# Kernel optimization log

Hardware: AMD Instinct MI355X
Metric: run time of the kernel (lower is better)

The kernel has to match this reference:

```python
import jax, jax.numpy as jnp
import numpy as np

N = 50000      # nodes
E = 1600000    # edges (avg degree 32)
DIN, DH, DOUT = 256, 128, 64


def gcn_conv(x, W, b, row, col, w, n):
    """One GCNConv layer (self-loops already appended to row/col/w).
    row = source nodes, col = target nodes; aggregate at targets."""
    xw = x @ W                                        # [n, d_out]
    deg = jax.ops.segment_sum(w, col, num_segments=n)  # in-degree weighted
    dinv = jnp.where(deg > 0, jax.lax.rsqrt(deg), 0.0)
    norm = dinv[row] * w * dinv[col]                  # [E+n]
    msg = norm[:, None] * xw[row]                     # [E+n, d_out] gather
    out = jax.ops.segment_sum(msg, col, num_segments=n)
    return out + b


def setup_inputs() -> dict:
    key = jax.random.key(0)
    k = jax.random.split(key, 6)
    x = jax.random.normal(k[0], (N, DIN), dtype=jnp.float32)
    edge_index = jax.random.randint(k[1], (2, E), 0, N)
    edge_weight = jax.random.uniform(k[2], (E,), dtype=jnp.float32)
    W1 = jax.random.normal(k[3], (DIN, DH), dtype=jnp.float32) * (1.0 / np.sqrt(DIN))
    b1 = jnp.zeros((DH,), dtype=jnp.float32)
    W2 = jax.random.normal(k[4], (DH, DOUT), dtype=jnp.float32) * (1.0 / np.sqrt(DH))
    b2 = jnp.zeros((DOUT,), dtype=jnp.float32)
    return {"x": x, "edge_index": edge_index, "edge_weight": edge_weight,
            "W1": W1, "b1": b1, "W2": W2, "b2": b2}


def reference(x, edge_index, edge_weight, W1, b1, W2, b2):
    n = x.shape[0]
    loops = jnp.arange(n, dtype=edge_index.dtype)
    row = jnp.concatenate([edge_index[0], loops])
    col = jnp.concatenate([edge_index[1], loops])
    w = jnp.concatenate([edge_weight, jnp.ones((n,), dtype=edge_weight.dtype)])
    h = gcn_conv(x, W1, b1, row, col, w, n)
    h = jax.nn.relu(h)
    # dropout(p=0.2) is identity in eval mode
    h = gcn_conv(h, W2, b2, row, col, w, n)
    return jax.nn.log_softmax(h, axis=-1)
```

## Files before the change

### kernel.cpp

```cpp
#include <hip/hip_runtime.h>
#include <hip/hip_bf16.h>
#include <cstddef>


#define DIN 256
#define DH  128
#define DOUT 64
#define NPB 100
#define NBMAX 512

typedef __bf16 bf16x8 __attribute__((ext_vector_type(8)));
typedef float f32x4 __attribute__((ext_vector_type(4)));

__device__ __forceinline__ float bflo(unsigned u) { return __uint_as_float(u << 16); }
__device__ __forceinline__ float bfhi(unsigned u) { return __uint_as_float(u & 0xffff0000u); }
__device__ __forceinline__ unsigned short f2bf(float f) {
    unsigned u = __float_as_uint(f);
    unsigned r = (u + 0x7fffu + ((u >> 16) & 1u)) >> 16;
    return (unsigned short)r;
}

__global__ void prep_w_kernel(const float* __restrict__ W1, const float* __restrict__ W2,
                              unsigned short* __restrict__ wt1, unsigned short* __restrict__ wt2) {
    int i = blockIdx.x * 256 + threadIdx.x;
    if (i < DH * DIN) {
        int nn = i >> 8, k = i & 255;
        wt1[i] = f2bf(W1[k * DH + nn]);
    } else {
        int j = i - DH * DIN;
        if (j < DOUT * DH) {
            int nn = j >> 7, k = j & 127;
            wt2[j] = f2bf(W2[k * DOUT + nn]);
        }
    }
}

__launch_bounds__(256)
__global__ void hist_kernel(const int* __restrict__ col, int* __restrict__ bh,
                            int E, int Ec, int NB) {
    __shared__ int hist[NBMAX];
    int p = blockIdx.x, t = threadIdx.x;
    for (int b = t; b < NB; b += 256) hist[b] = 0;
    __syncthreads();
    int s = p * Ec, e = min(s + Ec, E);
    for (int i = s + t; i < e; i += 256) atomicAdd(&hist[col[i] / NPB], 1);
    __syncthreads();
    for (int b = t; b < NB; b += 256) bh[p * NB + b] = hist[b];
}

__launch_bounds__(512)
__global__ void colscan_kernel(int* __restrict__ bh, int* __restrict__ btotal,
                               int P, int NB) {
    __shared__ int arr[512];
    int b = blockIdx.x, t = threadIdx.x;
    arr[t] = (t < P) ? bh[t * NB + b] : 0;
    __syncthreads();
    for (int off = 1; off < 512; off <<= 1) {
        int v = (t >= off) ? arr[t - off] : 0;
        __syncthreads();
        arr[t] += v;
        __syncthreads();
    }
    int excl = (t == 0) ? 0 : arr[t - 1];
    if (t < P) bh[t * NB + b] = excl;
    if (t == P - 1) btotal[b] = arr[t];
}

__launch_bounds__(512)
__global__ void basescan_kernel(const int* __restrict__ btotal, int* __restrict__ bbase,
                                int* __restrict__ rowptr, int NB, int n, int E) {
    __shared__ int arr[512];
    int t = threadIdx.x;
    arr[t] = (t < NB) ? btotal[t] : 0;
    __syncthreads();
    for (int off = 1; off < 512; off <<= 1) {
        int v = (t >= off) ? arr[t - off] : 0;
        __syncthreads();
        arr[t] += v;
        __syncthreads();
    }
    int excl = (t == 0) ? 0 : arr[t - 1];
    if (t <= NB) bbase[t] = excl;
    if (t == 511) rowptr[n] = E;
}

__launch_bounds__(256)
__global__ void scatter_kernel(const int* __restrict__ row, const int* __restrict__ col,
                               const float* __restrict__ w, const int* __restrict__ bh,
                               const int* __restrict__ bbase, int2* __restrict__ part,
                               int E, int Ec, int NB) {
    __shared__ int cur[NBMAX];
    int p = blockIdx.x, t = threadIdx.x;
    for (int b = t; b < NB; b += 256) cur[b] = bbase[b] + bh[p * NB + b];
    __syncthreads();
    int s = p * Ec, e = min(s + Ec, E);
    for (int i = s + t; i < e; i += 256) {
        int c = col[i];
        int r = row[i];
        int b = c / NPB;
        int pos = atomicAdd(&cur[b], 1);
        part[pos] = make_int2(r | ((c - b * NPB) << 16), __float_as_int(w[i]));
    }
}

__launch_bounds__(256)
__global__ void bucket_csr_kernel(const int2* __restrict__ part, const int* __restrict__ bbase,
                                  float* __restrict__ dinv, int* __restrict__ rowptr,
                                  int2* __restrict__ final_e, int n) {
    __shared__ int   hist[NPB];
    __shared__ float wsum[NPB];
    __shared__ int   nbase[NPB];
    __shared__ int   cur[NPB];
    int b = blockIdx.x, t = threadIdx.x;
    if (t < NPB) { hist[t] = 0; wsum[t] = 0.0f; }
    __syncthreads();
    int s = bbase[b], e = bbase[b + 1];
    for (int i = s + t; i < e; i += 256) {
        int2 rec = part[i];
        int cl = rec.x >> 16;
        atomicAdd(&hist[cl], 1);
        atomicAdd(&wsum[cl], __int_as_float(rec.y));
    }
    __syncthreads();
    if (t == 0) {
        int run = 0;
        for (int k = 0; k < NPB; ++k) { nbase[k] = run; run += hist[k]; }
    }
    __syncthreads();
    if (t < NPB) {
        int node = b * NPB + t;
        if (node < n) {
            dinv[node] = rsqrtf(1.0f + wsum[t]);
            rowptr[node] = s + nbase[t];
        }
        cur[t] = nbase[t];
    }
    __syncthreads();
    for (int i = s + t; i < e; i += 256) {
        int2 rec = part[i];
        int cl = rec.x >> 16;
        int q = s + atomicAdd(&cur[cl], 1);
        final_e[q] = make_int2(rec.x & 0xffff, rec.y);
    }
}

template <int K, int M>
__launch_bounds__(256)
__global__ void gemm_mfma_kernel(const float* __restrict__ A,
                                 const unsigned short* __restrict__ Wt,
                                 const float* __restrict__ scale,
                                 unsigned short* __restrict__ C, int N) {
    constexpr int BK = 64, LD = BK + 8;
    constexpr int WN = M / 4;
    constexpr int NT = WN / 16;
    constexpr int CLD = M + 8;
    constexpr int SM = (64 * LD + M * LD) > (64 * CLD) ? (64 * LD + M * LD) : (64 * CLD);
    __shared__ unsigned short smem[SM];
    __shared__ float sdv[64];
    unsigned short* As = smem;
    unsigned short* Bs = smem + 64 * LD;

    const int tid = threadIdx.x;
    const int row0 = blockIdx.x * 64;
    const int lane = tid & 63;
    const int quad = lane >> 4, r16 = lane & 15;
    const int n0 = (tid >> 6) * WN;

    if (tid < 64) {
        int r = row0 + tid;
        sdv[tid] = (r < N) ? scale[r] : 0.0f;
    }

    f32x4 acc[4][NT];
#pragma unroll
    for (int mt = 0; mt < 4; ++mt)
#pragma unroll
        for (int nt = 0; nt < NT; ++nt)
            acc[mt][nt] = (f32x4){0.f, 0.f, 0.f, 0.f};

    for (int k0 = 0; k0 < K; k0 += BK) {
#pragma unroll
        for (int j = 0; j < 4; ++j) {
            int idx = tid + j * 256;
            int m = idx >> 4;
            int q = idx & 15;
            int gr = row0 + m;
            float4 v = make_float4(0.f, 0.f, 0.f, 0.f);
            if (gr < N) v = *(const float4*)&A[(size_t)gr * K + k0 + q * 4];
            ushort4 s4;
            s4.x = f2bf(v.x); s4.y = f2bf(v.y); s4.z = f2bf(v.z); s4.w = f2bf(v.w);
            *(ushort4*)&As[m * LD + q * 4] = s4;
        }
#pragma unroll
        for (int j = 0; j < M * 8 / 256; ++j) {
            int idx = tid + j * 256;
            int nn = idx >> 3;
            int q = idx & 7;
            uint4 v = *(const uint4*)&Wt[(size_t)nn * K + k0 + q * 8];
            *(uint4*)&Bs[nn * LD + q * 8] = v;
        }
        __syncthreads();
#pragma unroll
        for (int ks = 0; ks < BK / 32; ++ks) {
            bf16x8 af[4], bfr[NT];
#pragma unroll
            for (int nt = 0; nt < NT; ++nt)
                bfr[nt] = *(const bf16x8*)&Bs[(n0 + nt * 16 + r16) * LD + ks * 32 + quad * 8];
#pragma unroll
            for (int mt = 0; mt < 4; ++mt)
                af[mt] = *(const bf16x8*)&As[(mt * 16 + r16) * LD + ks * 32 + quad * 8];
#pragma unroll
            for (int mt = 0; mt < 4; ++mt)
#pragma unroll
                for (int nt = 0; nt < NT; ++nt)
                    acc[mt][nt] = __builtin_amdgcn_mfma_f32_16x16x32_bf16(
                        af[mt], bfr[nt], acc[mt][nt], 0, 0, 0);
        }
        __syncthreads();
    }
    unsigned short* Cs = smem;
#pragma unroll
    for (int mt = 0; mt < 4; ++mt) {
#pragma unroll
        for (int i = 0; i < 4; ++i) {
            int r = mt * 16 + quad * 4 + i;
            float sc = sdv[r];
#pragma unroll
            for (int nt = 0; nt < NT; ++nt)
                Cs[r * CLD + n0 + nt * 16 + r16] = f2bf(acc[mt][nt][i] * sc);
        }
    }
    __syncthreads();
#pragma unroll
    for (int j = 0; j < 64 * M / 8 / 256; ++j) {
        int idx = tid + j * 256;
        int r = idx / (M / 8);
        int q = idx % (M / 8);
        int gr = row0 + r;
        if (gr < N) {
            uint4 v = *(const uint4*)&Cs[r * CLD + q * 8];
            *(uint4*)&C[(size_t)gr * M + q * 8] = v;
        }
    }
}

__launch_bounds__(256)
__global__ void agg1_kernel(const uint2* __restrict__ xw,
                            const int* __restrict__ rowptr,
                            const int2* __restrict__ edge,
                            const float* __restrict__ dinv,
                            const float* __restrict__ bias,
                            float* __restrict__ out, int n) {
    int node = blockIdx.x * 4 + (threadIdx.x >> 6);
    if (node >= n) return;
    int lane = threadIdx.x & 63;
    int half = lane >> 5, sub = lane & 31;
    float a0 = 0.f, a1 = 0.f, a2 = 0.f, a3 = 0.f;
    if (half == 0) {
        uint2 u = xw[(size_t)node * 32 + sub];
        a0 = bflo(u.x); a1 = bfhi(u.x); a2 = bflo(u.y); a3 = bfhi(u.y);
    }
    int p = rowptr[node], p1 = rowptr[node + 1];
    for (; p + 8 <= p1; p += 8) {
        int2 e0 = edge[p + half],     e1 = edge[p + 2 + half];
        int2 e2 = edge[p + 4 + half], e3 = edge[p + 6 + half];
        uint2 v0 = xw[(size_t)e0.x * 32 + sub];
        uint2 v1 = xw[(size_t)e1.x * 32 + sub];
        uint2 v2 = xw[(size_t)e2.x * 32 + sub];
        uint2 v3 = xw[(size_t)e3.x * 32 + sub];
        float w0 = __int_as_float(e0.y), w1 = __int_as_float(e1.y);
        float w2 = __int_as_float(e2.y), w3 = __int_as_float(e3.y);
        a0 += w0 * bflo(v0.x) + w1 * bflo(v1.x) + w2 * bflo(v2.x) + w3 * bflo(v3.x);
        a1 += w0 * bfhi(v0.x) + w1 * bfhi(v1.x) + w2 * bfhi(v2.x) + w3 * bfhi(v3.x);
        a2 += w0 * bflo(v0.y) + w1 * bflo(v1.y) + w2 * bflo(v2.y) + w3 * bflo(v3.y);
        a3 += w0 * bfhi(v0.y) + w1 * bfhi(v1.y) + w2 * bfhi(v2.y) + w3 * bfhi(v3.y);
    }
    for (; p + 2 <= p1; p += 2) {
        int2 e0 = edge[p + half];
        uint2 v0 = xw[(size_t)e0.x * 32 + sub];
        float w0 = __int_as_float(e0.y);
        a0 += w0 * bflo(v0.x); a1 += w0 * bfhi(v0.x);
        a2 += w0 * bflo(v0.y); a3 += w0 * bfhi(v0.y);
    }
    if (p < p1 && half == 0) {
        int2 e0 = edge[p];
        uint2 v0 = xw[(size_t)e0.x * 32 + sub];
        float w0 = __int_as_float(e0.y);
        a0 += w0 * bflo(v0.x); a1 += w0 * bfhi(v0.x);
        a2 += w0 * bflo(v0.y); a3 += w0 * bfhi(v0.y);
    }
    a0 += __shfl_xor(a0, 32); a1 += __shfl_xor(a1, 32);
    a2 += __shfl_xor(a2, 32); a3 += __shfl_xor(a3, 32);
    float di = dinv[node];
    float4 b = ((const float4*)bias)[sub];
    a0 = fmaxf(di * a0 + b.x, 0.f);
    a1 = fmaxf(di * a1 + b.y, 0.f);
    a2 = fmaxf(di * a2 + b.z, 0.f);
    a3 = fmaxf(di * a3 + b.w, 0.f);
    if (half == 0)
        ((float4*)out)[(size_t)node * 32 + sub] = make_float4(a0, a1, a2, a3);
}

__launch_bounds__(256)
__global__ void agg2_kernel(const uint2* __restrict__ xw,
                            const int* __restrict__ rowptr,
                            const int2* __restrict__ edge,
                            const float* __restrict__ dinv,
                            const float* __restrict__ bias,
                            float* __restrict__ out, int n) {
    int node = blockIdx.x * 4 + (threadIdx.x >> 6);
    if (node >= n) return;
    int lane = threadIdx.x & 63;
    int qw = lane >> 4, sub = lane & 15;
    float a0 = 0.f, a1 = 0.f, a2 = 0.f, a3 = 0.f;
    if (qw == 0) {
        uint2 u = xw[(size_t)node * 16 + sub];
        a0 = bflo(u.x); a1 = bfhi(u.x); a2 = bflo(u.y); a3 = bfhi(u.y);
    }
    int p = rowptr[node], p1 = rowptr[node + 1];
    for (; p + 8 <= p1; p += 8) {
        int2 e0 = edge[p + qw], e1 = edge[p + 4 + qw];
        uint2 v0 = xw[(size_t)e0.x * 16 + sub];
        uint2 v1 = xw[(size_t)e1.x * 16 + sub];
        float w0 = __int_as_float(e0.y), w1 = __int_as_float(e1.y);
        a0 += w0 * bflo(v0.x) + w1 * bflo(v1.x);
        a1 += w0 * bfhi(v0.x) + w1 * bfhi(v1.x);
        a2 += w0 * bflo(v0.y) + w1 * bflo(v1.y);
        a3 += w0 * bfhi(v0.y) + w1 * bfhi(v1.y);
    }
    for (; p + 4 <= p1; p += 4) {
        int2 e0 = edge[p + qw];
        uint2 v0 = xw[(size_t)e0.x * 16 + sub];
        float w0 = __int_as_float(e0.y);
        a0 += w0 * bflo(v0.x); a1 += w0 * bfhi(v0.x);
        a2 += w0 * bflo(v0.y); a3 += w0 * bfhi(v0.y);
    }
    int rem = p1 - p;
    if (qw < rem) {
        int2 e0 = edge[p + qw];
        uint2 v0 = xw[(size_t)e0.x * 16 + sub];
        float w0 = __int_as_float(e0.y);
        a0 += w0 * bflo(v0.x); a1 += w0 * bfhi(v0.x);
        a2 += w0 * bflo(v0.y); a3 += w0 * bfhi(v0.y);
    }
    a0 += __shfl_xor(a0, 32); a1 += __shfl_xor(a1, 32);
    a2 += __shfl_xor(a2, 32); a3 += __shfl_xor(a3, 32);
    a0 += __shfl_xor(a0, 16); a1 += __shfl_xor(a1, 16);
    a2 += __shfl_xor(a2, 16); a3 += __shfl_xor(a3, 16);
    float di = dinv[node];
    float4 b = ((const float4*)bias)[sub];
    a0 = di * a0 + b.x; a1 = di * a1 + b.y;
    a2 = di * a2 + b.z; a3 = di * a3 + b.w;
    float m = fmaxf(fmaxf(a0, a1), fmaxf(a2, a3));
#pragma unroll
    for (int off = 8; off > 0; off >>= 1) m = fmaxf(m, __shfl_xor(m, off));
    float s = __expf(a0 - m) + __expf(a1 - m) + __expf(a2 - m) + __expf(a3 - m);
#pragma unroll
    for (int off = 8; off > 0; off >>= 1) s += __shfl_xor(s, off);
    float lse = m + __logf(s);
    if (qw == 0)
        ((float4*)out)[(size_t)node * 16 + sub] =
            make_float4(a0 - lse, a1 - lse, a2 - lse, a3 - lse);
}

extern "C" void kernel_launch(void* const* d_in, const int* in_sizes, int n_in,
                              void* d_out, int out_size, void* d_ws, size_t ws_size,
                              hipStream_t stream) {
    const float* x  = (const float*)d_in[0];
    const int*   ei = (const int*)d_in[1];
    const float* ew = (const float*)d_in[2];
    const float* W1 = (const float*)d_in[3];
    const float* b1 = (const float*)d_in[4];
    const float* W2 = (const float*)d_in[5];
    const float* b2 = (const float*)d_in[6];
    float* out = (float*)d_out;

    const int n = in_sizes[0] / DIN;
    const int E = in_sizes[2];
    const int* row = ei;
    const int* col = ei + E;

    const int NB = (n + NPB - 1) / NPB;
    const int P  = NB;
    const int Ec = (E + P - 1) / P;

    char* ptr = (char*)d_ws;
    auto alloc = [&](size_t bytes) -> void* {
        void* r = (void*)ptr;
        ptr += (bytes + 255) & ~(size_t)255;
        return r;
    };
    int*   bh     = (int*)  alloc((size_t)P * NB * 4);
    int*   btotal = (int*)  alloc((size_t)NB * 4);
    int*   bbase  = (int*)  alloc((size_t)(NB + 1) * 4);
    int*   rowptr = (int*)  alloc((size_t)(n + 1) * 4);
    float* dinv   = (float*)alloc((size_t)n * 4);
    int2*  edge   = (int2*) alloc((size_t)E * 8);
    unsigned short* xw1 = (unsigned short*)alloc((size_t)n * DH * 2);
    unsigned short* wt1 = (unsigned short*)alloc((size_t)DH * DIN * 2);
    unsigned short* wt2 = (unsigned short*)alloc((size_t)DOUT * DH * 2);
    char* tail = (char*)alloc((size_t)n * DH * 4);
    int2*  part = (int2*)tail;
    float* h1   = (float*)tail;
    unsigned short* xw2 = xw1;

    const int nb_g = (n + 63) / 64;
    const int nb_a = (n + 3) / 4;

    prep_w_kernel<<<(DH * DIN + DOUT * DH + 255) / 256, 256, 0, stream>>>(W1, W2, wt1, wt2);
    hist_kernel<<<P, 256, 0, stream>>>(col, bh, E, Ec, NB);
    colscan_kernel<<<NB, 512, 0, stream>>>(bh, btotal, P, NB);
    basescan_kernel<<<1, 512, 0, stream>>>(btotal, bbase, rowptr, NB, n, E);
    scatter_kernel<<<P, 256, 0, stream>>>(row, col, ew, bh, bbase, part, E, Ec, NB);
    bucket_csr_kernel<<<NB, 256, 0, stream>>>(part, bbase, dinv, rowptr, edge, n);

    gemm_mfma_kernel<DIN, DH><<<nb_g, 256, 0, stream>>>(x, wt1, dinv, xw1, n);
    agg1_kernel<<<nb_a, 256, 0, stream>>>((const uint2*)xw1, rowptr, edge, dinv, b1, h1, n);
    gemm_mfma_kernel<DH, DOUT><<<nb_g, 256, 0, stream>>>(h1, wt2, dinv, xw2, n);
    agg2_kernel<<<nb_a, 256, 0, stream>>>((const uint2*)xw2, rowptr, edge, dinv, b2, out, n);
}
```

Before: 292.0 us.

## Widen aggregation gathers to 16-byte loads with prefetched edge records

Both aggregation kernels now have each lane gather 16-byte uint4 chunks (8 bf16 values) instead of 8-byte chunks. Each wavefront therefore processes more edges in parallel: 4 groups of 16 lanes in layer 1 and 8 groups of 8 lanes in layer 2. Edge records for the next iteration are prefetched while the current feature gathers are in flight. The tail is handled by clamped, padded loads that point at the node itself with zero weight instead of branching. The intent is fewer, wider memory transactions and more memory-level parallelism in these latency-bound gathers, at the cost of more registers, extra cross-lane shuffle reductions, and some wasted loads on padded tail edges.

Measured after the change: 282.5 us. 3.3% less time.

```diff
diff --git a/kernel.cpp b/kernel.cpp
--- a/kernel.cpp
+++ b/kernel.cpp
@@ -18,6 +18,13 @@
     unsigned u = __float_as_uint(f);
     unsigned r = (u + 0x7fffu + ((u >> 16) & 1u)) >> 16;
     return (unsigned short)r;
+}
+
+__device__ __forceinline__ int2 ldrec(const int2* __restrict__ e, int idx, int last, int fb) {
+    int ci = idx < last ? idx : last;
+    int2 r = e[ci];
+    if (idx > last) { r.x = fb; r.y = 0; }
+    return r;
 }
 
 __global__ void prep_w_kernel(const float* __restrict__ W1, const float* __restrict__ W2,
@@ -244,65 +251,14 @@
     }
 }
 
-__launch_bounds__(256)
-__global__ void agg1_kernel(const uint2* __restrict__ xw,
-                            const int* __restrict__ rowptr,
-                            const int2* __restrict__ edge,
-                            const float* __restrict__ dinv,
-                            const float* __restrict__ bias,
-                            float* __restrict__ out, int n) {
-    int node = blockIdx.x * 4 + (threadIdx.x >> 6);
-    if (node >= n) return;
-    int lane = threadIdx.x & 63;
-    int half = lane >> 5, sub = lane & 31;
-    float a0 = 0.f, a1 = 0.f, a2 = 0.f, a3 = 0.f;
-    if (half == 0) {
-        uint2 u = xw[(size_t)node * 32 + sub];
-        a0 = bflo(u.x); a1 = bfhi(u.x); a2 = bflo(u.y); a3 = bfhi(u.y);
-    }
-    int p = rowptr[node], p1 = rowptr[node + 1];
-    for (; p + 8 <= p1; p += 8) {
-        int2 e0 = edge[p + half],     e1 = edge[p + 2 + half];
-        int2 e2 = edge[p + 4 + half], e3 = edge[p + 6 + half];
-        uint2 v0 = xw[(size_t)e0.x * 32 + sub];
-        uint2 v1 = xw[(size_t)e1.x * 32 + sub];
-        uint2 v2 = xw[(size_t)e2.x * 32 + sub];
-        uint2 v3 = xw[(size_t)e3.x * 32 + sub];
-        float w0 = __int_as_float(e0.y), w1 = __int_as_float(e1.y);
-        float w2 = __int_as_float(e2.y), w3 = __int_as_float(e3.y);
-        a0 += w0 * bflo(v0.x) + w1 * bflo(v1.x) + w2 * bflo(v2.x) + w3 * bflo(v3.x);
-        a1 += w0 * bfhi(v0.x) + w1 * bfhi(v1.x) + w2 * bfhi(v2.x) + w3 * bfhi(v3.x);
-        a2 += w0 * bflo(v0.y) + w1 * bflo(v1.y) + w2 * bflo(v2.y) + w3 * bflo(v3.y);
-        a3 += w0 * bfhi(v0.y) + w1 * bfhi(v1.y) + w2 * bfhi(v2.y) + w3 * bfhi(v3.y);
-    }
-    for (; p + 2 <= p1; p += 2) {
-        int2 e0 = edge[p + half];
-        uint2 v0 = xw[(size_t)e0.x * 32 + sub];
-        float w0 = __int_as_float(e0.y);
-        a0 += w0 * bflo(v0.x); a1 += w0 * bfhi(v0.x);
-        a2 += w0 * bflo(v0.y); a3 += w0 * bfhi(v0.y);
-    }
-    if (p < p1 && half == 0) {
-        int2 e0 = edge[p];
-        uint2 v0 = xw[(size_t)e0.x * 32 + sub];
-        float w0 = __int_as_float(e0.y);
-        a0 += w0 * bflo(v0.x); a1 += w0 * bfhi(v0.x);
-        a2 += w0 * bflo(v0.y); a3 += w0 * bfhi(v0.y);
-    }
-    a0 += __shfl_xor(a0, 32); a1 += __shfl_xor(a1, 32);
-    a2 += __shfl_xor(a2, 32); a3 += __shfl_xor(a3, 32);
-    float di = dinv[node];
-    float4 b = ((const float4*)bias)[sub];
-    a0 = fmaxf(di * a0 + b.x, 0.f);
-    a1 = fmaxf(di * a1 + b.y, 0.f);
-    a2 = fmaxf(di * a2 + b.z, 0.f);
-    a3 = fmaxf(di * a3 + b.w, 0.f);
-    if (half == 0)
-        ((float4*)out)[(size_t)node * 32 + sub] = make_float4(a0, a1, a2, a3);
-}
-
-__launch_bounds__(256)
-__global__ void agg2_kernel(const uint2* __restrict__ xw,
+#define ACC8(v, wgt)                                            \
+    a0 += (wgt) * bflo((v).x); a1 += (wgt) * bfhi((v).x);       \
+    a2 += (wgt) * bflo((v).y); a3 += (wgt) * bfhi((v).y);       \
+    a4 += (wgt) * bflo((v).z); a5 += (wgt) * bfhi((v).z);       \
+    a6 += (wgt) * bflo((v).w); a7 += (wgt) * bfhi((v).w);
+
+__launch_bounds__(256, 8)
+__global__ void agg1_kernel(const unsigned short* __restrict__ xw,
                             const int* __restrict__ rowptr,
                             const int2* __restrict__ edge,
                             const float* __restrict__ dinv,
@@ -312,55 +268,168 @@
     if (node >= n) return;
     int lane = threadIdx.x & 63;
     int qw = lane >> 4, sub = lane & 15;
+    const char* xb = (const char*)xw;
+    const unsigned ssub = (unsigned)sub << 4;
+    float di = dinv[node];
+
     float a0 = 0.f, a1 = 0.f, a2 = 0.f, a3 = 0.f;
+    float a4 = 0.f, a5 = 0.f, a6 = 0.f, a7 = 0.f;
     if (qw == 0) {
-        uint2 u = xw[(size_t)node * 16 + sub];
+        uint4 u = *(const uint4*)(xb + (((unsigned)node) << 8) + ssub);
         a0 = bflo(u.x); a1 = bfhi(u.x); a2 = bflo(u.y); a3 = bfhi(u.y);
-    }
+        a4 = bflo(u.z); a5 = bfhi(u.z); a6 = bflo(u.w); a7 = bfhi(u.w);
+    }
+
     int p = rowptr[node], p1 = rowptr[node + 1];
-    for (; p + 8 <= p1; p += 8) {
-        int2 e0 = edge[p + qw], e1 = edge[p + 4 + qw];
-        uint2 v0 = xw[(size_t)e0.x * 16 + sub];
-        uint2 v1 = xw[(size_t)e1.x * 16 + sub];
+    int sbase = 4 * qw;
+    int2 ea, eb, ec, ed;
+    bool have = (p + 16 <= p1);
+    if (have) {
+        const int2* rp = edge + p + sbase;
+        ea = rp[0]; eb = rp[1]; ec = rp[2]; ed = rp[3];
+    }
+#pragma unroll 1
+    while (have) {
+        uint4 v0 = *(const uint4*)(xb + (((unsigned)ea.x) << 8) + ssub);
+        uint4 v1 = *(const uint4*)(xb + (((unsigned)eb.x) << 8) + ssub);
+        uint4 v2 = *(const uint4*)(xb + (((unsigned)ec.x) << 8) + ssub);
+        uint4 v3 = *(const uint4*)(xb + (((unsigned)ed.x) << 8) + ssub);
+        float w0 = __int_as_float(ea.y), w1 = __int_as_float(eb.y);
+        float w2 = __int_as_float(ec.y), w3 = __int_as_float(ed.y);
+        p += 16;
+        have = (p + 16 <= p1);
+        if (have) {
+            const int2* rp = edge + p + sbase;
+            ea = rp[0]; eb = rp[1]; ec = rp[2]; ed = rp[3];
+        }
+        ACC8(v0, w0); ACC8(v1, w1); ACC8(v2, w2); ACC8(v3, w3);
+    }
+    int rem = p1 - p;
+    if (rem > 0) {
+        int last = p1 - 1, b2 = p + sbase;
+        int2 e0 = ldrec(edge, b2, last, node);
+        int2 e1 = ldrec(edge, b2 + 1, last, node);
+        int2 e2 = ldrec(edge, b2 + 2, last, node);
+        int2 e3 = ldrec(edge, b2 + 3, last, node);
+        uint4 v0 = *(const uint4*)(xb + (((unsigned)e0.x) << 8) + ssub);
+        uint4 v1 = *(const uint4*)(xb + (((unsigned)e1.x) << 8) + ssub);
+        uint4 v2 = *(const uint4*)(xb + (((unsigned)e2.x) << 8) + ssub);
+        uint4 v3 = *(const uint4*)(xb + (((unsigned)e3.x) << 8) + ssub);
         float w0 = __int_as_float(e0.y), w1 = __int_as_float(e1.y);
-        a0 += w0 * bflo(v0.x) + w1 * bflo(v1.x);
-        a1 += w0 * bfhi(v0.x) + w1 * bfhi(v1.x);
-        a2 += w0 * bflo(v0.y) + w1 * bflo(v1.y);
-        a3 += w0 * bfhi(v0.y) + w1 * bfhi(v1.y);
-    }
-    for (; p + 4 <= p1; p += 4) {
-        int2 e0 = edge[p + qw];
-        uint2 v0 = xw[(size_t)e0.x * 16 + sub];
-        float w0 = __int_as_float(e0.y);
-        a0 += w0 * bflo(v0.x); a1 += w0 * bfhi(v0.x);
-        a2 += w0 * bflo(v0.y); a3 += w0 * bfhi(v0.y);
+        float w2 = __int_as_float(e2.y), w3 = __int_as_float(e3.y);
+        ACC8(v0, w0); ACC8(v1, w1); ACC8(v2, w2); ACC8(v3, w3);
+    }
+    a0 += __shfl_xor(a0, 16); a0 += __shfl_xor(a0, 32);
+    a1 += __shfl_xor(a1, 16); a1 += __shfl_xor(a1, 32);
+    a2 += __shfl_xor(a2, 16); a2 += __shfl_xor(a2, 32);
+    a3 += __shfl_xor(a3, 16); a3 += __shfl_xor(a3, 32);
+    a4 += __shfl_xor(a4, 16); a4 += __shfl_xor(a4, 32);
+    a5 += __shfl_xor(a5, 16); a5 += __shfl_xor(a5, 32);
+    a6 += __shfl_xor(a6, 16); a6 += __shfl_xor(a6, 32);
+    a7 += __shfl_xor(a7, 16); a7 += __shfl_xor(a7, 32);
+    if (qw < 2) {
+        float4 b = ((const float4*)bias)[2 * sub + qw];
+        float4 o = (qw == 0) ? make_float4(a0, a1, a2, a3)
+                             : make_float4(a4, a5, a6, a7);
+        o.x = fmaxf(di * o.x + b.x, 0.f);
+        o.y = fmaxf(di * o.y + b.y, 0.f);
+        o.z = fmaxf(di * o.z + b.z, 0.f);
+        o.w = fmaxf(di * o.w + b.w, 0.f);
+        ((float4*)out)[(size_t)node * 32 + 2 * sub + qw] = o;
+    }
+}
+
+__launch_bounds__(256, 8)
+__global__ void agg2_kernel(const unsigned short* __restrict__ xw,
+                            const int* __restrict__ rowptr,
+                            const int2* __restrict__ edge,
+                            const float* __restrict__ dinv,
+                            const float* __restrict__ bias,
+                            float* __restrict__ out, int n) {
+    int node = blockIdx.x * 4 + (threadIdx.x >> 6);
+    if (node >= n) return;
+    int lane = threadIdx.x & 63;
+    int oct = lane >> 3, sub = lane & 7;
+    const char* xb = (const char*)xw;
+    const unsigned ssub = (unsigned)sub << 4;
+    float di = dinv[node];
+
+    float a0 = 0.f, a1 = 0.f, a2 = 0.f, a3 = 0.f;
+    float a4 = 0.f, a5 = 0.f, a6 = 0.f, a7 = 0.f;
+    if (oct == 0) {
+        uint4 u = *(const uint4*)(xb + (((unsigned)node) << 7) + ssub);
+        a0 = bflo(u.x); a1 = bfhi(u.x); a2 = bflo(u.y); a3 = bfhi(u.y);
+        a4 = bflo(u.z); a5 = bfhi(u.z); a6 = bflo(u.w); a7 = bfhi(u.w);
+    }
+
+    int p = rowptr[node], p1 = rowptr[node + 1];
+    int sbase = 4 * oct;
+    int2 ea, eb, ec, ed;
+    bool have = (p + 32 <= p1);
+    if (have) {
+        const int2* rp = edge + p + sbase;
+        ea = rp[0]; eb = rp[1]; ec = rp[2]; ed = rp[3];
+    }
+#pragma unroll 1
+    while (have) {
+        uint4 v0 = *(const uint4*)(xb + (((unsigned)ea.x) << 7) + ssub);
+        uint4 v1 = *(const uint4*)(xb + (((unsigned)eb.x) << 7) + ssub);
+        uint4 v2 = *(const uint4*)(xb + (((unsigned)ec.x) << 7) + ssub);
+        uint4 v3 = *(const uint4*)(xb + (((unsigned)ed.x) << 7) + ssub);
+        float w0 = __int_as_float(ea.y), w1 = __int_as_float(eb.y);
+        float w2 = __int_as_float(ec.y), w3 = __int_as_float(ed.y);
+        p += 32;
+        have = (p + 32 <= p1);
+        if (have) {
+            const int2* rp = edge + p + sbase;
+            ea = rp[0]; eb = rp[1]; ec = rp[2]; ed = rp[3];
+        }
+        ACC8(v0, w0); ACC8(v1, w1); ACC8(v2, w2); ACC8(v3, w3);
     }
     int rem = p1 - p;
-    if (qw < rem) {
-        int2 e0 = edge[p + qw];
-        uint2 v0 = xw[(size_t)e0.x * 16 + sub];
-        float w0 = __int_as_float(e0.y);
-        a0 += w0 * bflo(v0.x); a1 += w0 * bfhi(v0.x);
-        a2 += w0 * bflo(v0.y); a3 += w0 * bfhi(v0.y);
-    }
-    a0 += __shfl_xor(a0, 32); a1 += __shfl_xor(a1, 32);
-    a2 += __shfl_xor(a2, 32); a3 += __shfl_xor(a3, 32);
-    a0 += __shfl_xor(a0, 16); a1 += __shfl_xor(a1, 16);
-    a2 += __shfl_xor(a2, 16); a3 += __shfl_xor(a3, 16);
-    float di = dinv[node];
-    float4 b = ((const float4*)bias)[sub];
-    a0 = di * a0 + b.x; a1 = di * a1 + b.y;
-    a2 = di * a2 + b.z; a3 = di * a3 + b.w;
-    float m = fmaxf(fmaxf(a0, a1), fmaxf(a2, a3));
-#pragma unroll
-    for (int off = 8; off > 0; off >>= 1) m = fmaxf(m, __shfl_xor(m, off));
-    float s = __expf(a0 - m) + __expf(a1 - m) + __expf(a2 - m) + __expf(a3 - m);
-#pragma unroll
-    for (int off = 8; off > 0; off >>= 1) s += __shfl_xor(s, off);
+    if (rem > 0) {
+        int last = p1 - 1, b2 = p + sbase;
+        int2 e0 = ldrec(edge, b2, last, node);
+        int2 e1 = ldrec(edge, b2 + 1, last, node);
+        int2 e2 = ldrec(edge, b2 + 2, last, node);
+        int2 e3 = ldrec(edge, b2 + 3, last, node);
+        uint4 v0 = *(const uint4*)(xb + (((unsigned)e0.x) << 7) + ssub);
+        uint4 v1 = *(const uint4*)(xb + (((unsigned)e1.x) << 7) + ssub);
+        uint4 v2 = *(const uint4*)(xb + (((unsigned)e2.x) << 7) + ssub);
+        uint4 v3 = *(const uint4*)(xb + (((unsigned)e3.x) << 7) + ssub);
+        float w0 = __int_as_float(e0.y), w1 = __int_as_float(e1.y);
+        float w2 = __int_as_float(e2.y), w3 = __int_as_float(e3.y);
+        ACC8(v0, w0); ACC8(v1, w1); ACC8(v2, w2); ACC8(v3, w3);
+    }
+    a0 += __shfl_xor(a0, 8); a0 += __shfl_xor(a0, 16); a0 += __shfl_xor(a0, 32);
+    a1 += __shfl_xor(a1, 8); a1 += __shfl_xor(a1, 16); a1 += __shfl_xor(a1, 32);
+    a2 += __shfl_xor(a2, 8); a2 += __shfl_xor(a2, 16); a2 += __shfl_xor(a2, 32);
+    a3 += __shfl_xor(a3, 8); a3 += __shfl_xor(a3, 16); a3 += __shfl_xor(a3, 32);
+    a4 += __shfl_xor(a4, 8); a4 += __shfl_xor(a4, 16); a4 += __shfl_xor(a4, 32);
+    a5 += __shfl_xor(a5, 8); a5 += __shfl_xor(a5, 16); a5 += __shfl_xor(a5, 32);
+    a6 += __shfl_xor(a6, 8); a6 += __shfl_xor(a6, 16); a6 += __shfl_xor(a6, 32);
+    a7 += __shfl_xor(a7, 8); a7 += __shfl_xor(a7, 16); a7 += __shfl_xor(a7, 32);
+    const float4* bp = (const float4*)bias;
+    float4 bl = bp[2 * sub], bh = bp[2 * sub + 1];
+    a0 = di * a0 + bl.x; a1 = di * a1 + bl.y; a2 = di * a2 + bl.z; a3 = di * a3 + bl.w;
+    a4 = di * a4 + bh.x; a5 = di * a5 + bh.y; a6 = di * a6 + bh.z; a7 = di * a7 + bh.w;
+    float m = fmaxf(fmaxf(fmaxf(a0, a1), fmaxf(a2, a3)),
+                    fmaxf(fmaxf(a4, a5), fmaxf(a6, a7)));
+    m = fmaxf(m, __shfl_xor(m, 4));
+    m = fmaxf(m, __shfl_xor(m, 2));
+    m = fmaxf(m, __shfl_xor(m, 1));
+    float s = __expf(a0 - m) + __expf(a1 - m) + __expf(a2 - m) + __expf(a3 - m)
+            + __expf(a4 - m) + __expf(a5 - m) + __expf(a6 - m) + __expf(a7 - m);
+    s += __shfl_xor(s, 4);
+    s += __shfl_xor(s, 2);
+    s += __shfl_xor(s, 1);
     float lse = m + __logf(s);
-    if (qw == 0)
-        ((float4*)out)[(size_t)node * 16 + sub] =
-            make_float4(a0 - lse, a1 - lse, a2 - lse, a3 - lse);
+    if (oct < 2) {
+        float4 o = (oct == 0) ? make_float4(a0, a1, a2, a3)
+                              : make_float4(a4, a5, a6, a7);
+        ((float4*)out)[(size_t)node * 16 + 2 * sub + oct] =
+            make_float4(o.x - lse, o.y - lse, o.z - lse, o.w - lse);
+    }
 }
 
 extern "C" void kernel_launch(void* const* d_in, const int* in_sizes, int n_in,
@@ -415,7 +484,7 @@
     bucket_csr_kernel<<<NB, 256, 0, stream>>>(part, bbase, dinv, rowptr, edge, n);
 
     gemm_mfma_kernel<DIN, DH><<<nb_g, 256, 0, stream>>>(x, wt1, dinv, xw1, n);
-    agg1_kernel<<<nb_a, 256, 0, stream>>>((const uint2*)xw1, rowptr, edge, dinv, b1, h1, n);
+    agg1_kernel<<<nb_a, 256, 0, stream>>>(xw1, rowptr, edge, dinv, b1, h1, n);
     gemm_mfma_kernel<DH, DOUT><<<nb_g, 256, 0, stream>>>(h1, wt2, dinv, xw2, n);
-    agg2_kernel<<<nb_a, 256, 0, stream>>>((const uint2*)xw2, rowptr, edge, dinv, b2, out, n);
-}
+    agg2_kernel<<<nb_a, 256, 0, stream>>>(xw2, rowptr, edge, dinv, b2, out, n);
+}
```

## Slice aggregation by feature columns and pack edges into 32-bit records

Applied to the files above, without the earlier changes.

Edge records are compressed to 4 bytes each: a 16-bit source index plus a 16-bit fp16 weight. Aggregation is split into per-column-slice passes (4 for layer 1, 2 for layer 2). In each pass a wave handles 16 edges at once, with 4 lanes per edge and 16 bytes per lane, and the next edge record is prefetched. The aim is to shrink the gather working set per pass so it fits in cache, and to halve edge-list traffic. In exchange the edge list is re-read on every pass, log-softmax moves into a separate kernel, and the fp16 weights add rounding.

After: 357.7 us. 1.23x slower.

```diff
diff --git a/kernel.cpp b/kernel.cpp
--- a/kernel.cpp
+++ b/kernel.cpp
@@ -1,5 +1,6 @@
 #include <hip/hip_runtime.h>
 #include <hip/hip_bf16.h>
+#include <hip/hip_fp16.h>
 #include <cstddef>
 
 
@@ -106,7 +107,7 @@
 __launch_bounds__(256)
 __global__ void bucket_csr_kernel(const int2* __restrict__ part, const int* __restrict__ bbase,
                                   float* __restrict__ dinv, int* __restrict__ rowptr,
-                                  int2* __restrict__ final_e, int n) {
+                                  unsigned* __restrict__ final_e, int n) {
     __shared__ int   hist[NPB];
     __shared__ float wsum[NPB];
     __shared__ int   nbase[NPB];
@@ -140,7 +141,8 @@
         int2 rec = part[i];
         int cl = rec.x >> 16;
         int q = s + atomicAdd(&cur[cl], 1);
-        final_e[q] = make_int2(rec.x & 0xffff, rec.y);
+        unsigned short ws = __half_as_ushort(__float2half_rn(__int_as_float(rec.y)));
+        final_e[q] = ((unsigned)rec.x & 0xffffu) | ((unsigned)ws << 16);
     }
 }
 
@@ -244,123 +246,92 @@
     }
 }
 
-__launch_bounds__(256)
-__global__ void agg1_kernel(const uint2* __restrict__ xw,
+template <int ROWSHIFT, bool RELU>
+__launch_bounds__(256, 8)
+__global__ void aggs_kernel(const unsigned short* __restrict__ xw,
                             const int* __restrict__ rowptr,
-                            const int2* __restrict__ edge,
+                            const unsigned* __restrict__ edge,
                             const float* __restrict__ dinv,
                             const float* __restrict__ bias,
-                            float* __restrict__ out, int n) {
+                            float* __restrict__ out, int n, int pslice) {
+    constexpr int OUTV4 = (1 << ROWSHIFT) / 8;
     int node = blockIdx.x * 4 + (threadIdx.x >> 6);
     if (node >= n) return;
     int lane = threadIdx.x & 63;
-    int half = lane >> 5, sub = lane & 31;
+    int slot = lane >> 2, q = lane & 3;
+    const char* xb = (const char*)xw;
+    const unsigned soff = (unsigned)pslice * 64 + (unsigned)q * 16;
+
     float a0 = 0.f, a1 = 0.f, a2 = 0.f, a3 = 0.f;
-    if (half == 0) {
-        uint2 u = xw[(size_t)node * 32 + sub];
+    float a4 = 0.f, a5 = 0.f, a6 = 0.f, a7 = 0.f;
+    if (slot == 0) {
+        uint4 u = *(const uint4*)(xb + (((unsigned)node) << ROWSHIFT) + soff);
         a0 = bflo(u.x); a1 = bfhi(u.x); a2 = bflo(u.y); a3 = bfhi(u.y);
-    }
-    int p = rowptr[node], p1 = rowptr[node + 1];
-    for (; p + 8 <= p1; p += 8) {
-        int2 e0 = edge[p + half],     e1 = edge[p + 2 + half];
-        int2 e2 = edge[p + 4 + half], e3 = edge[p + 6 + half];
-        uint2 v0 = xw[(size_t)e0.x * 32 + sub];
-        uint2 v1 = xw[(size_t)e1.x * 32 + sub];
-        uint2 v2 = xw[(size_t)e2.x * 32 + sub];
-        uint2 v3 = xw[(size_t)e3.x * 32 + sub];
-        float w0 = __int_as_float(e0.y), w1 = __int_as_float(e1.y);
-        float w2 = __int_as_float(e2.y), w3 = __int_as_float(e3.y);
-        a0 += w0 * bflo(v0.x) + w1 * bflo(v1.x) + w2 * bflo(v2.x) + w3 * bflo(v3.x);
-        a1 += w0 * bfhi(v0.x) + w1 * bfhi(v1.x) + w2 * bfhi(v2.x) + w3 * bfhi(v3.x);
-        a2 += w0 * bflo(v0.y) + w1 * bflo(v1.y) + w2 * bflo(v2.y) + w3 * bflo(v3.y);
-        a3 += w0 * bfhi(v0.y) + w1 * bfhi(v1.y) + w2 * bfhi(v2.y) + w3 * bfhi(v3.y);
-    }
-    for (; p + 2 <= p1; p += 2) {
-        int2 e0 = edge[p + half];
-        uint2 v0 = xw[(size_t)e0.x * 32 + sub];
-        float w0 = __int_as_float(e0.y);
-        a0 += w0 * bflo(v0.x); a1 += w0 * bfhi(v0.x);
-        a2 += w0 * bflo(v0.y); a3 += w0 * bfhi(v0.y);
-    }
-    if (p < p1 && half == 0) {
-        int2 e0 = edge[p];
-        uint2 v0 = xw[(size_t)e0.x * 32 + sub];
-        float w0 = __int_as_float(e0.y);
-        a0 += w0 * bflo(v0.x); a1 += w0 * bfhi(v0.x);
-        a2 += w0 * bflo(v0.y); a3 += w0 * bfhi(v0.y);
-    }
-    a0 += __shfl_xor(a0, 32); a1 += __shfl_xor(a1, 32);
-    a2 += __shfl_xor(a2, 32); a3 += __shfl_xor(a3, 32);
-    float di = dinv[node];
-    float4 b = ((const float4*)bias)[sub];
-    a0 = fmaxf(di * a0 + b.x, 0.f);
-    a1 = fmaxf(di * a1 + b.y, 0.f);
-    a2 = fmaxf(di * a2 + b.z, 0.f);
-    a3 = fmaxf(di * a3 + b.w, 0.f);
-    if (half == 0)
-        ((float4*)out)[(size_t)node * 32 + sub] = make_float4(a0, a1, a2, a3);
-}
-
-__launch_bounds__(256)
-__global__ void agg2_kernel(const uint2* __restrict__ xw,
-                            const int* __restrict__ rowptr,
-                            const int2* __restrict__ edge,
-                            const float* __restrict__ dinv,
-                            const float* __restrict__ bias,
-                            float* __restrict__ out, int n) {
-    int node = blockIdx.x * 4 + (threadIdx.x >> 6);
+        a4 = bflo(u.z); a5 = bfhi(u.z); a6 = bflo(u.w); a7 = bfhi(u.w);
+    }
+
+    int p0 = rowptr[node], p1 = rowptr[node + 1];
+    int last = p1 - 1;
+    int nr = (p1 - p0 + 15) >> 4;
+    int idx = p0 + slot;
+    unsigned rec = edge[(idx <= last) ? idx : ((last >= 0) ? last : 0)];
+#pragma unroll 1
+    for (int r = 0; r < nr; ++r) {
+        bool on = idx <= last;
+        unsigned src = rec & 0xffffu;
+        float w = on ? __half2float(__ushort_as_half((unsigned short)(rec >> 16))) : 0.0f;
+        uint4 v = *(const uint4*)(xb + (src << ROWSHIFT) + soff);
+        idx += 16;
+        int ns = (idx <= last) ? idx : ((last >= 0) ? last : 0);
+        rec = edge[ns];
+        a0 += w * bflo(v.x); a1 += w * bfhi(v.x);
+        a2 += w * bflo(v.y); a3 += w * bfhi(v.y);
+        a4 += w * bflo(v.z); a5 += w * bfhi(v.z);
+        a6 += w * bflo(v.w); a7 += w * bfhi(v.w);
+    }
+#define REDSL(x) x += __shfl_xor(x, 4); x += __shfl_xor(x, 8); \
+                 x += __shfl_xor(x, 16); x += __shfl_xor(x, 32);
+    REDSL(a0) REDSL(a1) REDSL(a2) REDSL(a3)
+    REDSL(a4) REDSL(a5) REDSL(a6) REDSL(a7)
+#undef REDSL
+    if (slot == 0) {
+        float di = dinv[node];
+        const float4* bp = (const float4*)bias;
+        float4 b0 = bp[pslice * 8 + q * 2], b1 = bp[pslice * 8 + q * 2 + 1];
+        float4 o0 = make_float4(di * a0 + b0.x, di * a1 + b0.y,
+                                di * a2 + b0.z, di * a3 + b0.w);
+        float4 o1 = make_float4(di * a4 + b1.x, di * a5 + b1.y,
+                                di * a6 + b1.z, di * a7 + b1.w);
+        if (RELU) {
+            o0.x = fmaxf(o0.x, 0.f); o0.y = fmaxf(o0.y, 0.f);
+            o0.z = fmaxf(o0.z, 0.f); o0.w = fmaxf(o0.w, 0.f);
+            o1.x = fmaxf(o1.x, 0.f); o1.y = fmaxf(o1.y, 0.f);
+            o1.z = fmaxf(o1.z, 0.f); o1.w = fmaxf(o1.w, 0.f);
+        }
+        ((float4*)out)[(size_t)node * OUTV4 + pslice * 8 + q * 2]     = o0;
+        ((float4*)out)[(size_t)node * OUTV4 + pslice * 8 + q * 2 + 1] = o1;
+    }
+}
+
+__launch_bounds__(256, 8)
+__global__ void lsm_kernel(float* __restrict__ out, int n) {
+    int node = blockIdx.x * 16 + (threadIdx.x >> 4);
     if (node >= n) return;
-    int lane = threadIdx.x & 63;
-    int qw = lane >> 4, sub = lane & 15;
-    float a0 = 0.f, a1 = 0.f, a2 = 0.f, a3 = 0.f;
-    if (qw == 0) {
-        uint2 u = xw[(size_t)node * 16 + sub];
-        a0 = bflo(u.x); a1 = bfhi(u.x); a2 = bflo(u.y); a3 = bfhi(u.y);
-    }
-    int p = rowptr[node], p1 = rowptr[node + 1];
-    for (; p + 8 <= p1; p += 8) {
-        int2 e0 = edge[p + qw], e1 = edge[p + 4 + qw];
-        uint2 v0 = xw[(size_t)e0.x * 16 + sub];
-        uint2 v1 = xw[(size_t)e1.x * 16 + sub];
-        float w0 = __int_as_float(e0.y), w1 = __int_as_float(e1.y);
-        a0 += w0 * bflo(v0.x) + w1 * bflo(v1.x);
-        a1 += w0 * bfhi(v0.x) + w1 * bfhi(v1.x);
-        a2 += w0 * bflo(v0.y) + w1 * bflo(v1.y);
-        a3 += w0 * bfhi(v0.y) + w1 * bfhi(v1.y);
-    }
-    for (; p + 4 <= p1; p += 4) {
-        int2 e0 = edge[p + qw];
-        uint2 v0 = xw[(size_t)e0.x * 16 + sub];
-        float w0 = __int_as_float(e0.y);
-        a0 += w0 * bflo(v0.x); a1 += w0 * bfhi(v0.x);
-        a2 += w0 * bflo(v0.y); a3 += w0 * bfhi(v0.y);
-    }
-    int rem = p1 - p;
-    if (qw < rem) {
-        int2 e0 = edge[p + qw];
-        uint2 v0 = xw[(size_t)e0.x * 16 + sub];
-        float w0 = __int_as_float(e0.y);
-        a0 += w0 * bflo(v0.x); a1 += w0 * bfhi(v0.x);
-        a2 += w0 * bflo(v0.y); a3 += w0 * bfhi(v0.y);
-    }
-    a0 += __shfl_xor(a0, 32); a1 += __shfl_xor(a1, 32);
-    a2 += __shfl_xor(a2, 32); a3 += __shfl_xor(a3, 32);
-    a0 += __shfl_xor(a0, 16); a1 += __shfl_xor(a1, 16);
-    a2 += __shfl_xor(a2, 16); a3 += __shfl_xor(a3, 16);
-    float di = dinv[node];
-    float4 b = ((const float4*)bias)[sub];
-    a0 = di * a0 + b.x; a1 = di * a1 + b.y;
-    a2 = di * a2 + b.z; a3 = di * a3 + b.w;
-    float m = fmaxf(fmaxf(a0, a1), fmaxf(a2, a3));
-#pragma unroll
-    for (int off = 8; off > 0; off >>= 1) m = fmaxf(m, __shfl_xor(m, off));
-    float s = __expf(a0 - m) + __expf(a1 - m) + __expf(a2 - m) + __expf(a3 - m);
-#pragma unroll
-    for (int off = 8; off > 0; off >>= 1) s += __shfl_xor(s, off);
-    float lse = m + __logf(s);
-    if (qw == 0)
-        ((float4*)out)[(size_t)node * 16 + sub] =
-            make_float4(a0 - lse, a1 - lse, a2 - lse, a3 - lse);
+    int s = threadIdx.x & 15;
+    float4 v = ((const float4*)out)[(size_t)node * 16 + s];
+    float m = fmaxf(fmaxf(v.x, v.y), fmaxf(v.z, v.w));
+    m = fmaxf(m, __shfl_xor(m, 1));
+    m = fmaxf(m, __shfl_xor(m, 2));
+    m = fmaxf(m, __shfl_xor(m, 4));
+    m = fmaxf(m, __shfl_xor(m, 8));
+    float e = __expf(v.x - m) + __expf(v.y - m) + __expf(v.z - m) + __expf(v.w - m);
+    e += __shfl_xor(e, 1);
+    e += __shfl_xor(e, 2);
+    e += __shfl_xor(e, 4);
+    e += __shfl_xor(e, 8);
+    float lse = m + __logf(e);
+    ((float4*)out)[(size_t)node * 16 + s] =
+        make_float4(v.x - lse, v.y - lse, v.z - lse, v.w - lse);
 }
 
 extern "C" void kernel_launch(void* const* d_in, const int* in_sizes, int n_in,
@@ -395,7 +366,7 @@
     int*   bbase  = (int*)  alloc((size_t)(NB + 1) * 4);
     int*   rowptr = (int*)  alloc((size_t)(n + 1) * 4);
     float* dinv   = (float*)alloc((size_t)n * 4);
-    int2*  edge   = (int2*) alloc((size_t)E * 8);
+    unsigned* edge = (unsigned*)alloc((size_t)E * 4);
     unsigned short* xw1 = (unsigned short*)alloc((size_t)n * DH * 2);
     unsigned short* wt1 = (unsigned short*)alloc((size_t)DH * DIN * 2);
     unsigned short* wt2 = (unsigned short*)alloc((size_t)DOUT * DH * 2);
@@ -406,6 +377,7 @@
 
     const int nb_g = (n + 63) / 64;
     const int nb_a = (n + 3) / 4;
+    const int nb_s = (n + 15) / 16;
 
     prep_w_kernel<<<(DH * DIN + DOUT * DH + 255) / 256, 256, 0, stream>>>(W1, W2, wt1, wt2);
     hist_kernel<<<P, 256, 0, stream>>>(col, bh, E, Ec, NB);
@@ -415,7 +387,10 @@
     bucket_csr_kernel<<<NB, 256, 0, stream>>>(part, bbase, dinv, rowptr, edge, n);
 
     gemm_mfma_kernel<DIN, DH><<<nb_g, 256, 0, stream>>>(x, wt1, dinv, xw1, n);
-    agg1_kernel<<<nb_a, 256, 0, stream>>>((const uint2*)xw1, rowptr, edge, dinv, b1, h1, n);
+    for (int p = 0; p < 4; ++p)
+        aggs_kernel<8, true><<<nb_a, 256, 0, stream>>>(xw1, rowptr, edge, dinv, b1, h1, n, p);
     gemm_mfma_kernel<DH, DOUT><<<nb_g, 256, 0, stream>>>(h1, wt2, dinv, xw2, n);
-    agg2_kernel<<<nb_a, 256, 0, stream>>>((const uint2*)xw2, rowptr, edge, dinv, b2, out, n);
-}
+    for (int p = 0; p < 2; ++p)
+        aggs_kernel<7, false><<<nb_a, 256, 0, stream>>>(xw2, rowptr, edge, dinv, b2, out, n, p);
+    lsm_kernel<<<nb_s, 256, 0, stream>>>(out, n);
+}
```
